# Performance work log

Measured on AMD Instinct MI355X. Metric: run time of the kernel, lower is better.

Reference implementation:

```python
import jax, jax.numpy as jnp
import numpy as np

DIM = 512
B, H_GRID, W_GRID = 16, 64, 64
N_TOKENS = 1 + H_GRID * W_GRID


def setup_inputs() -> dict:
    key = jax.random.key(0)
    ks = jax.random.split(key, 7)
    x = jax.random.normal(ks[0], (B, N_TOKENS, DIM), dtype=jnp.float32)
    # depthwise conv weights, torch layout [C_out, C_in/groups=1, k, k]
    w7 = jax.random.normal(ks[1], (DIM, 1, 7, 7), dtype=jnp.float32) * 0.02
    b7 = jax.random.normal(ks[2], (DIM,), dtype=jnp.float32) * 0.02
    w5 = jax.random.normal(ks[3], (DIM, 1, 5, 5), dtype=jnp.float32) * 0.02
    b5 = jax.random.normal(ks[4], (DIM,), dtype=jnp.float32) * 0.02
    w3 = jax.random.normal(ks[5], (DIM, 1, 3, 3), dtype=jnp.float32) * 0.02
    b3 = jax.random.normal(ks[6], (DIM,), dtype=jnp.float32) * 0.02
    return {"x": x, "w7": w7, "b7": b7, "w5": w5, "b5": b5,
            "w3": w3, "b3": b3, "H": H_GRID, "W": W_GRID}


def _dwconv(v, w, b, k):
    # depthwise same-padding conv, NCHW / OIHW, feature_group_count = channels
    p = k // 2
    C = v.shape[1]
    y = jax.lax.conv_general_dilated(
        v, w, window_strides=(1, 1), padding=[(p, p), (p, p)],
        dimension_numbers=("NCHW", "OIHW", "NCHW"),
        feature_group_count=C)
    return y + b[None, :, None, None]


def reference(x, w7, b7, w5, b5, w3, b3, H, W):
    Bsz, N, C = x.shape
    cls_token = x[:, :1]                         # [B, 1, C]
    feat_tokens = x[:, 1:]                       # [B, H*W, C]
    cnn_feat = feat_tokens.transpose(0, 2, 1).reshape(Bsz, C, H, W)
    x_conv = (_dwconv(cnn_feat, w7, b7, 7)
              + _dwconv(cnn_feat, w5, b5, 5)
              + _dwconv(cnn_feat, w3, b3, 3)
              + cnn_feat)
    feats = x_conv.reshape(Bsz, C, H * W).transpose(0, 2, 1)  # [B, H*W, C]
    return jnp.concatenate((cls_token, feats), axis=1)
```

## Files before the change

kernel.cpp:

```cpp
#include <hip/hip_runtime.h>

#define DIMC 512
#define NTOK 4097
#define GH 64
#define GW 64
#define TH 16

__global__ __launch_bounds__(256) void prep_kernel(
    const float* __restrict__ w7, const float* __restrict__ b7,
    const float* __restrict__ w5, const float* __restrict__ b5,
    const float* __restrict__ w3, const float* __restrict__ b3,
    float* __restrict__ wc, float* __restrict__ bc)
{
    int idx = blockIdx.x * 256 + threadIdx.x;
    if (idx < DIMC * 49) {
        int c = idx & (DIMC - 1);
        int t = idx >> 9;
        int dy = t / 7, dx = t - dy * 7;
        float v = w7[c * 49 + t];
        if (dy >= 1 && dy <= 5 && dx >= 1 && dx <= 5)
            v += w5[c * 25 + (dy - 1) * 5 + (dx - 1)];
        if (dy >= 2 && dy <= 4 && dx >= 2 && dx <= 4)
            v += w3[c * 9 + (dy - 2) * 3 + (dx - 2)];
        if (dy == 3 && dx == 3) v += 1.0f;
        wc[t * DIMC + c] = v;
    }
    if (idx < DIMC) bc[idx] = b7[idx] + b5[idx] + b3[idx];
}

__global__ __launch_bounds__(256) void cls_kernel(
    const float* __restrict__ x, float* __restrict__ out)
{
    int i = blockIdx.x * 256 + threadIdx.x;
    int b = i >> 9, c = i & 511;
    size_t off = (size_t)b * NTOK * DIMC + c;
    out[off] = x[off];
}

__global__ __launch_bounds__(256) void dwconv_kernel(
    const float* __restrict__ x, const float* __restrict__ wc,
    const float* __restrict__ bc, float* __restrict__ out)
{
    const int c_in_chunk = threadIdx.x;
    const int wlane = threadIdx.y;
    const int wseg = blockIdx.x;
    const int yid  = blockIdx.y;
    const int b    = blockIdx.z;
    const int cc = (yid >> 2) * 64 + c_in_chunk;
    const int h0 = (yid & 3) * TH;
    const int w  = wseg * 4 + wlane;

    float wgt[49];
#pragma unroll
    for (int t = 0; t < 49; ++t) wgt[t] = wc[t * DIMC + cc];
    const float bias = bc[cc];

    const float* __restrict__ xin = x   + ((size_t)b * NTOK + 1) * DIMC + cc;
    float* __restrict__ op        = out + ((size_t)b * NTOK + 1) * DIMC + cc;

    float win[7][7];

    auto load_row = [&](int r, float* row) {
        if (r < 0 || r >= GH) {
#pragma unroll
            for (int dx = 0; dx < 7; ++dx) row[dx] = 0.0f;
        } else {
            const float* rp = xin + (size_t)r * GW * DIMC;
#pragma unroll
            for (int dx = 0; dx < 7; ++dx) {
                int col = w - 3 + dx;
                row[dx] = (col >= 0 && col < GW) ? rp[(size_t)col * DIMC] : 0.0f;
            }
        }
    };

#pragma unroll
    for (int p = 0; p < 6; ++p) load_row(h0 - 3 + p, win[p]);

#pragma unroll
    for (int o = 0; o < TH; ++o) {
        load_row(h0 + o + 3, win[(o + 6) % 7]);
        float acc = bias;
#pragma unroll
        for (int dy = 0; dy < 7; ++dy) {
            const float* row = win[(o + dy) % 7];
#pragma unroll
            for (int dx = 0; dx < 7; ++dx)
                acc += wgt[dy * 7 + dx] * row[dx];
        }
        op[((size_t)(h0 + o) * GW + w) * DIMC] = acc;
    }
}

extern "C" void kernel_launch(void* const* d_in, const int* in_sizes, int n_in,
                              void* d_out, int out_size, void* d_ws, size_t ws_size,
                              hipStream_t stream)
{
    const float* x  = (const float*)d_in[0];
    const float* w7 = (const float*)d_in[1];
    const float* b7 = (const float*)d_in[2];
    const float* w5 = (const float*)d_in[3];
    const float* b5 = (const float*)d_in[4];
    const float* w3 = (const float*)d_in[5];
    const float* b3 = (const float*)d_in[6];
    float* out = (float*)d_out;
    float* wcomb = (float*)d_ws;
    float* bcomb = wcomb + 49 * DIMC;

    prep_kernel<<<98, 256, 0, stream>>>(w7, b7, w5, b5, w3, b3, wcomb, bcomb);
    cls_kernel<<<32, 256, 0, stream>>>(x, out);

    dim3 grid(16, 32, 16);
    dim3 block(64, 4, 1);
    dwconv_kernel<<<grid, block, 0, stream>>>(x, wcomb, bcomb, out);
}
```

Before: 346.2 us.

## Register-tile four output columns per thread to reuse loaded rows

Each thread now computes a 16x4 output tile instead of a single column. It streams input rows of width 10 once and accumulates each into a rolling set of seven partial-sum rows. This reduces redundant global/cache loads across neighboring columns and quarters the grid size. In exchange it raises register pressure, which launch bounds try to keep within four blocks per CU, and it reduces parallelism.

New measurement: 397.8 us. 1.15x slower.

```diff
diff --git a/kernel.cpp b/kernel.cpp
--- a/kernel.cpp
+++ b/kernel.cpp
@@ -5,6 +5,7 @@
 #define GH 64
 #define GW 64
 #define TH 16
+#define WT 4
 
 __global__ __launch_bounds__(256) void prep_kernel(
     const float* __restrict__ w7, const float* __restrict__ b7,
@@ -37,18 +38,17 @@
     out[off] = x[off];
 }
 
-__global__ __launch_bounds__(256) void dwconv_kernel(
+__global__ __launch_bounds__(256, 4) void dwconv_kernel(
     const float* __restrict__ x, const float* __restrict__ wc,
     const float* __restrict__ bc, float* __restrict__ out)
 {
-    const int c_in_chunk = threadIdx.x;
-    const int wlane = threadIdx.y;
-    const int wseg = blockIdx.x;
-    const int yid  = blockIdx.y;
-    const int b    = blockIdx.z;
-    const int cc = (yid >> 2) * 64 + c_in_chunk;
-    const int h0 = (yid & 3) * TH;
-    const int w  = wseg * 4 + wlane;
+    const int lane  = threadIdx.x;
+    const int wtile = threadIdx.y;
+    const int b     = blockIdx.z;
+    const int cg    = blockIdx.y >> 2;
+    const int h0    = (blockIdx.y & 3) * TH;
+    const int w0    = (blockIdx.x * 4 + wtile) * WT;
+    const int cc    = (cg << 6) + lane;
 
     float wgt[49];
 #pragma unroll
@@ -58,37 +58,48 @@
     const float* __restrict__ xin = x   + ((size_t)b * NTOK + 1) * DIMC + cc;
     float* __restrict__ op        = out + ((size_t)b * NTOK + 1) * DIMC + cc;
 
-    float win[7][7];
+    float acc[7][WT];
+    float row[WT + 6];
 
-    auto load_row = [&](int r, float* row) {
-        if (r < 0 || r >= GH) {
 #pragma unroll
-            for (int dx = 0; dx < 7; ++dx) row[dx] = 0.0f;
+    for (int i = 0; i < TH + 6; ++i) {
+        const int r = h0 - 3 + i;
+
+        if (r >= 0 && r < GH) {
+            const float* __restrict__ rp = xin + (size_t)r * (GW * DIMC);
+#pragma unroll
+            for (int j = 0; j < WT + 6; ++j) {
+                const int col = w0 - 3 + j;
+                row[j] = (col >= 0 && col < GW) ? rp[(size_t)col * DIMC] : 0.0f;
+            }
         } else {
-            const float* rp = xin + (size_t)r * GW * DIMC;
 #pragma unroll
-            for (int dx = 0; dx < 7; ++dx) {
-                int col = w - 3 + dx;
-                row[dx] = (col >= 0 && col < GW) ? rp[(size_t)col * DIMC] : 0.0f;
+            for (int j = 0; j < WT + 6; ++j) row[j] = 0.0f;
+        }
+
+#pragma unroll
+        for (int dy = 0; dy < 7; ++dy) {
+            const int k = i - dy;
+            if (k < 0 || k >= TH) continue;
+            const int s = k % 7;
+#pragma unroll
+            for (int t = 0; t < WT; ++t) {
+                float a = (dy == 0) ? bias : acc[s][t];
+#pragma unroll
+                for (int dx = 0; dx < 7; ++dx)
+                    a = fmaf(wgt[dy * 7 + dx], row[t + dx], a);
+                acc[s][t] = a;
             }
         }
-    };
 
+        if (i >= 6) {
+            const int k = i - 6;
+            const int s = k % 7;
+            const size_t ro = (size_t)(h0 + k) * GW;
 #pragma unroll
-    for (int p = 0; p < 6; ++p) load_row(h0 - 3 + p, win[p]);
-
-#pragma unroll
-    for (int o = 0; o < TH; ++o) {
-        load_row(h0 + o + 3, win[(o + 6) % 7]);
-        float acc = bias;
-#pragma unroll
-        for (int dy = 0; dy < 7; ++dy) {
-            const float* row = win[(o + dy) % 7];
-#pragma unroll
-            for (int dx = 0; dx < 7; ++dx)
-                acc += wgt[dy * 7 + dx] * row[dx];
+            for (int t = 0; t < WT; ++t)
+                op[(ro + (w0 + t)) * DIMC] = acc[s][t];
         }
-        op[((size_t)(h0 + o) * GW + w) * DIMC] = acc;
     }
 }
 
@@ -110,7 +121,7 @@
     prep_kernel<<<98, 256, 0, stream>>>(w7, b7, w5, b5, w3, b3, wcomb, bcomb);
     cls_kernel<<<32, 256, 0, stream>>>(x, out);
 
-    dim3 grid(16, 32, 16);
+    dim3 grid(4, 32, 16);
     dim3 block(64, 4, 1);
     dwconv_kernel<<<grid, block, 0, stream>>>(x, wcomb, bcomb, out);
 }
```
